# Optimization experiments

Measured on AMD Instinct MI355X. Metric: run time of the kernel, lower is better.

## Reference

```python
import jax, jax.numpy as jnp
import numpy as np

K_N = 20          # neighbors (init kwarg k_n)
EPS = 1e-5        # BN / InstanceNorm eps (torch default)


def _conv1x1(x, w, b):
    # x: [B,C,N,K], w: [O,C], b: [O]
    return jnp.einsum('bcnk,oc->bonk', x, w) + b[None, :, None, None]


def _bn(x, g, b):
    # training-mode BatchNorm2d: stats over (B,N,K)
    mean = x.mean(axis=(0, 2, 3), keepdims=True)
    var = x.var(axis=(0, 2, 3), keepdims=True)
    return (x - mean) * jax.lax.rsqrt(var + EPS) * g[None, :, None, None] + b[None, :, None, None]


def _inorm(x):
    # InstanceNorm2d (affine=False): stats over (N,K) per (b,c)
    mean = x.mean(axis=(2, 3), keepdims=True)
    var = x.var(axis=(2, 3), keepdims=True)
    return (x - mean) * jax.lax.rsqrt(var + EPS)


def _knn(x, k):
    # x: [B,C,N] -> idx [B,N,k] of nearest neighbors (excluding self)
    sq = jnp.sum(x * x, axis=1)                                   # [B,N]
    neg_d = 2.0 * jnp.einsum('bcn,bcm->bnm', x, x) - sq[:, :, None] - sq[:, None, :]
    _, idx = jax.lax.top_k(neg_d, k + 1)
    return idx[:, :, 1:]


def _res_block(x, w1, b1, g1, be1, w2, b2, g2, be2):
    # pre=False: residual branch is identity
    out = jax.nn.relu(_bn(_inorm(_conv1x1(x, w1, b1)), g1, be1))
    out = _bn(_inorm(_conv1x1(out, w2, b2)), g2, be2)
    return jax.nn.relu(out + x)


def _forward(data, conv0_w, conv0_b, bn0_g, bn0_b, lin_w, lin_b,
             res_w1, res_b1, res_g1, res_be1, res_w2, res_b2, res_g2, res_be2):
    B, C, N = data.shape
    # graph_feature: degree feature from normalized affinity matrix
    nrm = jnp.linalg.norm(data, axis=1, keepdims=True) + 1e-5
    o = data / nrm
    A = jnp.einsum('bcn,bcm->bnm', o, o)                          # [B,N,N]
    D = (jnp.sum(A, axis=1, keepdims=True) - 1.0) / N             # [B,1,N] (subtract eye diag)
    feat = jnp.concatenate([data, jax.nn.relu(jnp.tanh(D))], axis=1)  # [B,129,N]

    idx = _knn(feat, K_N)                                         # [B,N,k]
    xt = jnp.transpose(feat, (0, 2, 1))                           # [B,N,129]
    gathered = jax.vmap(lambda xb, ib: xb[ib])(xt, idx)           # [B,N,k,129]
    center = xt[:, :, None, :]
    edge = jnp.concatenate([jnp.broadcast_to(center, gathered.shape),
                            center - gathered], axis=3)           # [B,N,k,258]
    edge = jnp.transpose(edge, (0, 3, 1, 2))                      # [B,258,N,k]

    out = jax.nn.relu(_bn(_conv1x1(edge, conv0_w, conv0_b), bn0_g, bn0_b))
    out = jnp.max(out, axis=3, keepdims=True)                     # max_pool2d (1,k) -> [B,128,N,1]
    for i in range(4):
        out = _res_block(out, res_w1[i], res_b1[i], res_g1[i], res_be1[i],
                         res_w2[i], res_b2[i], res_g2[i], res_be2[i])
    logit = _conv1x1(out, lin_w, lin_b)                           # [B,1,N,1]
    return logit.reshape(logit.shape[0], -1)                      # [B,N]


def setup_inputs() -> dict:
    B, C, N = 8, 128, 2048
    key = jax.random.key(0)
    ks = jax.random.split(key, 10)
    s = 0.05
    return {
        'data': jax.random.normal(ks[0], (B, C, N), dtype=jnp.float32),
        'x': jax.random.normal(ks[1], (B, C, N), dtype=jnp.float32),  # unused by module
        'conv0_w': jax.random.normal(ks[2], (128, 258), dtype=jnp.float32) * s,
        'conv0_b': jnp.zeros((128,), dtype=jnp.float32),
        'bn0_g': jnp.ones((128,), dtype=jnp.float32),
        'bn0_b': jnp.zeros((128,), dtype=jnp.float32),
        'lin_w': jax.random.normal(ks[3], (1, 128), dtype=jnp.float32) * s,
        'lin_b': jnp.zeros((1,), dtype=jnp.float32),
        'res_w1': jax.random.normal(ks[4], (4, 128, 128), dtype=jnp.float32) * s,
        'res_b1': jnp.zeros((4, 128), dtype=jnp.float32),
        'res_g1': jnp.ones((4, 128), dtype=jnp.float32),
        'res_be1': jnp.zeros((4, 128), dtype=jnp.float32),
        'res_w2': jax.random.normal(ks[5], (4, 128, 128), dtype=jnp.float32) * s,
        'res_b2': jnp.zeros((4, 128), dtype=jnp.float32),
        'res_g2': jnp.ones((4, 128), dtype=jnp.float32),
        'res_be2': jnp.zeros((4, 128), dtype=jnp.float32),
    }


def reference(data, x, conv0_w, conv0_b, bn0_g, bn0_b, lin_w, lin_b,
              res_w1, res_b1, res_g1, res_be1, res_w2, res_b2, res_g2, res_be2):
    # x is accepted but unused, matching the torch module
    return _forward(data, conv0_w, conv0_b, bn0_g, bn0_b, lin_w, lin_b,
                    res_w1, res_b1, res_g1, res_be1, res_w2, res_b2, res_g2, res_be2)
```

## Files before the change

kernel.cpp:

```cpp
#include <hip/hip_runtime.h>
#include <math.h>
#include <float.h>

#define NB 8
#define NC 128
#define NN 2048
#define KNN 20
#define CF 129
#define CFP 144
#define EPSV 1e-5f

#define S_OFF      0
#define BN0S_OFF   1024
#define RESST_OFF  1280
#define NRM_OFF    17664
#define ZERO_CNT   34048
#define SQN_OFF    34048
#define WCAT_OFF   50432
#define FEAT_OFF   103936
#define PQ_OFF     2463232
#define X_OFF      6657536
#define SLOT_SZ    2097152
#define IDX_OFF    12948992
#define G_OFF      13276672
#define XB_OFF     46831104
#define WS_FLOATS  48928256
#define MMN_OFF    (X_OFF + SLOT_SZ)
#define MMX_OFF    (X_OFF + 2 * SLOT_SZ)

__launch_bounds__(256)
__global__ void k1a_sq(const float* __restrict__ data, float* __restrict__ ws) {
    int b = blockIdx.y;
    int n = blockIdx.x * 256 + threadIdx.x;
    int c0 = blockIdx.z * 32;
    const float* dp = data + (size_t)b * NC * NN + (size_t)c0 * NN + n;
    float acc = 0.f;
#pragma unroll
    for (int c = 0; c < 32; ++c) { float v = dp[(size_t)c * NN]; acc = fmaf(v, v, acc); }
    atomicAdd(&ws[NRM_OFF + b * NN + n], acc);
}

__launch_bounds__(256)
__global__ void k1s_colsum(const float* __restrict__ data, float* __restrict__ ws) {
    int b = blockIdx.y;
    int c0 = blockIdx.x * 16;
    int tid = threadIdx.x, w = tid >> 6, lane = tid & 63;
    __shared__ float Linv[NN];
    for (int r = tid; r < NN; r += 256)
        Linv[r] = 1.f / (sqrtf(ws[NRM_OFF + b * NN + r]) + 1e-5f);
    __syncthreads();
#pragma unroll
    for (int i = 0; i < 4; ++i) {
        int c = c0 + w * 4 + i;
        const float* dp = data + (size_t)b * NC * NN + (size_t)c * NN;
        float acc = 0.f;
        for (int n = lane; n < NN; n += 64) acc = fmaf(dp[n], Linv[n], acc);
        for (int off = 32; off; off >>= 1) acc += __shfl_down(acc, off);
        if (lane == 0) ws[S_OFF + b * NC + c] = acc;
    }
}

__launch_bounds__(256)
__global__ void k2_feat(const float* __restrict__ data, float* __restrict__ ws) {
    int b = blockIdx.y;
    int n0 = blockIdx.x * 64;
    int tid = threadIdx.x;
    __shared__ float Sb[NC];
    __shared__ __align__(16) float fT[64][CFP];
    __shared__ float redD[4][64], redQ[4][64];
    if (tid < NC) Sb[tid] = ws[S_OFF + b * NC + tid];
    __syncthreads();
    int nn = tid & 63, cg = tid >> 6;
    float dotp = 0.f, sq = 0.f;
    const float* dp = data + (size_t)b * NC * NN + n0 + nn;
    for (int c = cg; c < NC; c += 4) {
        float v = dp[(size_t)c * NN];
        fT[nn][c] = v;
        dotp += Sb[c] * v;
        sq += v * v;
    }
    redD[cg][nn] = dotp; redQ[cg][nn] = sq;
    __syncthreads();
    if (tid < 64) {
        float dt = redD[0][tid] + redD[1][tid] + redD[2][tid] + redD[3][tid];
        float sv = redQ[0][tid] + redQ[1][tid] + redQ[2][tid] + redQ[3][tid];
        float nrm = sqrtf(ws[NRM_OFF + b * NN + n0 + tid]) + 1e-5f;
        float D = (dt / nrm - 1.f) * (1.f / (float)NN);
        float f1 = tanhf(D); if (f1 < 0.f) f1 = 0.f;
        fT[tid][NC] = f1;
        for (int c = NC + 1; c < CFP; ++c) fT[tid][c] = 0.f;
        ws[SQN_OFF + b * NN + n0 + tid] = sv + f1 * f1;
    }
    __syncthreads();
    float* out = ws + FEAT_OFF + (size_t)(b * NN + n0) * CFP;
    for (int i = tid; i < 64 * CFP; i += 256) out[i] = ((float*)fT)[i];
}

__launch_bounds__(256)
__global__ void k4_wcat(const float* __restrict__ w, float* __restrict__ ws) {
    int i = blockIdx.x * 256 + threadIdx.x;
    int o = i / CFP, c = i % CFP;
    float v = 0.f;
    if (c < CF) {
        if (o < 128) v = w[o * 258 + c] + w[o * 258 + CF + c];
        else         v = w[(o - 128) * 258 + CF + c];
    }
    ws[WCAT_OFF + i] = v;
}

__launch_bounds__(256)
__global__ void k3_gram(float* __restrict__ ws) {
    __shared__ __align__(16) float As[8][128];
    __shared__ __align__(16) float Bs[8][128];
    int tid = threadIdx.x;
    int b = blockIdx.z;
    int m0 = blockIdx.x * 128, n0 = blockIdx.y * 128;
    const float* F = ws + FEAT_OFF + (size_t)b * NN * CFP;
    float acc[8][8];
#pragma unroll
    for (int i = 0; i < 8; ++i)
#pragma unroll
        for (int j = 0; j < 8; ++j) acc[i][j] = 0.f;
    int rr = tid >> 1, cq = tid & 1;
    int tx = tid & 15, ty = tid >> 4;
    for (int kc = 0; kc < CFP; kc += 8) {
        float4 av = *(const float4*)&F[(size_t)(n0 + rr) * CFP + kc + cq * 4];
        float4 bv = *(const float4*)&F[(size_t)(m0 + rr) * CFP + kc + cq * 4];
        __syncthreads();
        As[cq*4+0][rr] = av.x; As[cq*4+1][rr] = av.y; As[cq*4+2][rr] = av.z; As[cq*4+3][rr] = av.w;
        Bs[cq*4+0][rr] = bv.x; Bs[cq*4+1][rr] = bv.y; Bs[cq*4+2][rr] = bv.z; Bs[cq*4+3][rr] = bv.w;
        __syncthreads();
#pragma unroll
        for (int kk = 0; kk < 8; ++kk) {
            float a[8], bb[8];
            *(float4*)&a[0]  = *(const float4*)&As[kk][ty * 8];
            *(float4*)&a[4]  = *(const float4*)&As[kk][ty * 8 + 4];
            *(float4*)&bb[0] = *(const float4*)&Bs[kk][tx * 4];
            *(float4*)&bb[4] = *(const float4*)&Bs[kk][64 + tx * 4];
#pragma unroll
            for (int i = 0; i < 8; ++i)
#pragma unroll
                for (int j = 0; j < 8; ++j) acc[i][j] = fmaf(a[i], bb[j], acc[i][j]);
        }
    }
    float sqv[8];
#pragma unroll
    for (int j = 0; j < 4; ++j) {
        sqv[j]     = ws[SQN_OFF + b * NN + m0 + tx * 4 + j];
        sqv[4 + j] = ws[SQN_OFF + b * NN + m0 + 64 + tx * 4 + j];
    }
    float* G = ws + G_OFF + (size_t)b * NN * NN;
#pragma unroll
    for (int i = 0; i < 8; ++i) {
        int row = n0 + ty * 8 + i;
        float4 o1, o2;
        o1.x = 2.f*acc[i][0]-sqv[0]; o1.y = 2.f*acc[i][1]-sqv[1];
        o1.z = 2.f*acc[i][2]-sqv[2]; o1.w = 2.f*acc[i][3]-sqv[3];
        o2.x = 2.f*acc[i][4]-sqv[4]; o2.y = 2.f*acc[i][5]-sqv[5];
        o2.z = 2.f*acc[i][6]-sqv[6]; o2.w = 2.f*acc[i][7]-sqv[7];
        *(float4*)&G[(size_t)row * NN + m0 + tx * 4]      = o1;
        *(float4*)&G[(size_t)row * NN + m0 + 64 + tx * 4] = o2;
    }
}

__launch_bounds__(256)
__global__ void ksel(float* __restrict__ ws) {
    int wid = threadIdx.x >> 6, lane = threadIdx.x & 63;
    int r = blockIdx.x * 4 + wid;
    const float* row = ws + G_OFF + (size_t)r * NN;
    float v[32];
#pragma unroll
    for (int i = 0; i < 32; ++i) v[i] = row[lane + (i << 6)];
    float b1v = -FLT_MAX, b2v = -FLT_MAX;
    int b1i = 0, b2i = 0;
#pragma unroll
    for (int i = 0; i < 32; ++i) {
        float x = v[i];
        if (x > b1v)      { b2v = b1v; b2i = b1i; b1v = x; b1i = i; }
        else if (x > b2v) { b2v = x; b2i = i; }
    }
    unsigned int mask = 0u;
    bool has2 = true;
    int* out = (int*)(ws + IDX_OFF) + (size_t)r * KNN;
    for (int k = 0; k < 21; ++k) {
        float M = b1v;
#pragma unroll
        for (int off = 1; off < 64; off <<= 1) M = fmaxf(M, __shfl_xor(M, off));
        unsigned long long tied = __ballot(b1v == M);
        int mm;
        if (__popcll(tied) > 1) {
            int cand = (b1v == M) ? ((b1i << 6) | lane) : 0x7FFFFFFF;
#pragma unroll
            for (int off = 1; off < 64; off <<= 1) {
                int oc = __shfl_xor(cand, off);
                cand = oc < cand ? oc : cand;
            }
            mm = cand;
        } else {
            int l = __ffsll(tied) - 1;
            mm = (__shfl(b1i, l) << 6) | l;
        }
        if (k > 0 && lane == 0) out[k - 1] = mm;
        if (lane == (mm & 63)) {
            mask |= 1u << b1i;
            if (has2) { b1v = b2v; b1i = b2i; has2 = false; }
            else {
                b1v = -FLT_MAX; b2v = -FLT_MAX; b1i = 0; b2i = 0;
#pragma unroll
                for (int i = 0; i < 32; ++i) {
                    float x = (mask & (1u << i)) ? -FLT_MAX : v[i];
                    if (x > b1v)      { b2v = b1v; b2i = b1i; b1v = x; b1i = i; }
                    else if (x > b2v) { b2v = x; b2i = i; }
                }
                has2 = true;
            }
        }
    }
}

__launch_bounds__(256)
__global__ void k5_pq(float* __restrict__ ws) {
    __shared__ __align__(16) float As[16][64];
    __shared__ __align__(16) float Bs[16][64];
    int tid = threadIdx.x;
    int m0 = blockIdx.x * 64, o0 = blockIdx.y * 64;
    int rr = tid >> 2, cq = tid & 3;
    int tx = tid & 15, ty = tid >> 4;
    float acc[4][4];
#pragma unroll
    for (int i = 0; i < 4; ++i)
#pragma unroll
        for (int j = 0; j < 4; ++j) acc[i][j] = 0.f;
    const float* F  = ws + FEAT_OFF;
    const float* Wc = ws + WCAT_OFF;
    for (int kc = 0; kc < CFP; kc += 16) {
        float4 av = *(const float4*)&F [(size_t)(m0 + rr) * CFP + kc + cq * 4];
        float4 bv = *(const float4*)&Wc[(size_t)(o0 + rr) * CFP + kc + cq * 4];
        __syncthreads();
        As[cq*4+0][rr]=av.x; As[cq*4+1][rr]=av.y; As[cq*4+2][rr]=av.z; As[cq*4+3][rr]=av.w;
        Bs[cq*4+0][rr]=bv.x; Bs[cq*4+1][rr]=bv.y; Bs[cq*4+2][rr]=bv.z; Bs[cq*4+3][rr]=bv.w;
        __syncthreads();
#pragma unroll
        for (int kk = 0; kk < 16; ++kk) {
            float a[4], bb[4];
            *(float4*)&a[0]  = *(const float4*)&As[kk][ty * 4];
            *(float4*)&bb[0] = *(const float4*)&Bs[kk][tx * 4];
#pragma unroll
            for (int i = 0; i < 4; ++i)
#pragma unroll
                for (int j = 0; j < 4; ++j) acc[i][j] = fmaf(a[i], bb[j], acc[i][j]);
        }
    }
#pragma unroll
    for (int i = 0; i < 4; ++i) {
        float4 o;
        o.x = acc[i][0]; o.y = acc[i][1]; o.z = acc[i][2]; o.w = acc[i][3];
        *(float4*)&ws[PQ_OFF + (size_t)(m0 + ty * 4 + i) * 256 + o0 + tx * 4] = o;
    }
}

__launch_bounds__(256)
__global__ void k6_bn0stats(float* __restrict__ ws) {
    int tid = threadIdx.x;
    int o = tid & 127, h = tid >> 7;
    int m0 = blockIdx.x * 16;
    const float* PQ = ws + PQ_OFF;
    const int* idx = (const int*)(ws + IDX_OFF);
    float* MMn = ws + MMN_OFF;
    float* MMx = ws + MMX_OFF;
    __shared__ float red[2][128];
    float s = 0.f, q = 0.f;
    for (int p = h; p < 16; p += 2) {
        int m = m0 + p;
        int bb = m >> 11;
        float pv = PQ[(size_t)m * 256 + o];
        const int* ip = idx + (size_t)m * KNN;
        float mn = FLT_MAX, mx = -FLT_MAX;
        for (int k = 0; k < KNN; ++k) {
            int j = ip[k];
            float val = pv - PQ[(size_t)(bb * NN + j) * 256 + 128 + o];
            s += val; q += val * val;
            mn = fminf(mn, val); mx = fmaxf(mx, val);
        }
        MMn[(size_t)m * NC + o] = mn;
        MMx[(size_t)m * NC + o] = mx;
    }
    red[h][o] = s; __syncthreads();
    if (tid < 128) atomicAdd(&ws[BN0S_OFF + tid], red[0][tid] + red[1][tid]);
    __syncthreads();
    red[h][o] = q; __syncthreads();
    if (tid < 128) atomicAdd(&ws[BN0S_OFF + 128 + tid], red[0][tid] + red[1][tid]);
}

__launch_bounds__(256)
__global__ void k8_apply(float* __restrict__ ws, const float* __restrict__ g,
                         const float* __restrict__ be) {
    int e = blockIdx.x * 256 + threadIdx.x;
    int fi = e * 4;
    int o = fi & 127;
    const float cnt = 1.f / (float)(NB * NN * KNN);
    float4 sum4 = *(const float4*)&ws[BN0S_OFF + o];
    float4 ssq4 = *(const float4*)&ws[BN0S_OFF + 128 + o];
    float4 g4   = *(const float4*)&g[o];
    float4 be4  = *(const float4*)&be[o];
    float4 mn = *(const float4*)&ws[MMN_OFF + fi];
    float4 mx = *(const float4*)&ws[MMX_OFF + fi];
    float4 r;
#define BN0_DO(comp) { \
    float m_ = sum4.comp * cnt; \
    float v_ = ssq4.comp * cnt - m_ * m_; if (v_ < 0.f) v_ = 0.f; \
    float sc_ = g4.comp * rsqrtf(v_ + EPSV); \
    float sh_ = be4.comp - m_ * sc_; \
    r.comp = fmaxf(fmaf(sc_ > 0.f ? mx.comp : mn.comp, sc_, sh_), 0.f); }
    BN0_DO(x) BN0_DO(y) BN0_DO(z) BN0_DO(w)
#undef BN0_DO
    *(float4*)&ws[X_OFF + fi] = r;
}

__launch_bounds__(256)
__global__ void k9f_conv(const float* __restrict__ x, const float* __restrict__ w,
                         float* __restrict__ y, float* __restrict__ stats,
                         const float* __restrict__ statsIn,
                         const float* __restrict__ g, const float* __restrict__ be,
                         const float* __restrict__ xin, float* __restrict__ xw) {
    __shared__ __align__(16) float As[16][64];
    __shared__ __align__(16) float Bs[16][64];
    __shared__ float red[16][64];
    __shared__ float vvv[8][128];
    __shared__ float scs[128], shs[128];
    int tid = threadIdx.x;
    int m0 = blockIdx.x * 64, o0 = blockIdx.y * 64;
    int bA = m0 >> 11;
    if (statsIn) {
        for (int e = tid; e < 1024; e += 256) {
            float sum = statsIn[e], ssq = statsIn[1024 + e];
            float m_ = sum * (1.f / (float)NN);
            float v_ = ssq * (1.f / (float)NN) - m_ * m_; if (v_ < 0.f) v_ = 0.f;
            vvv[e >> 7][e & 127] = v_ / (v_ + EPSV);
        }
        __syncthreads();
        if (tid < 128) {
            float a = 0.f;
#pragma unroll
            for (int b2 = 0; b2 < NB; ++b2) a += vvv[b2][tid];
            float rsbn = rsqrtf(a * (1.f / (float)NB) + EPSV);
            float sum = statsIn[bA * 128 + tid], ssq = statsIn[1024 + bA * 128 + tid];
            float m_ = sum * (1.f / (float)NN);
            float v_ = ssq * (1.f / (float)NN) - m_ * m_; if (v_ < 0.f) v_ = 0.f;
            float sc_ = rsqrtf(v_ + EPSV) * rsbn * g[tid];
            scs[tid] = sc_;
            shs[tid] = be[tid] - m_ * sc_;
        }
        __syncthreads();
    }
    int rr = tid >> 2, cq = tid & 3;
    int tx = tid & 15, ty = tid >> 4;
    float acc[4][4];
#pragma unroll
    for (int i = 0; i < 4; ++i)
#pragma unroll
        for (int j = 0; j < 4; ++j) acc[i][j] = 0.f;
    for (int kc = 0; kc < NC; kc += 16) {
        float4 av = *(const float4*)&x[(size_t)(m0 + rr) * NC + kc + cq * 4];
        if (statsIn) {
            int c = kc + cq * 4;
            av.x = fmaf(av.x, scs[c],     shs[c]);
            av.y = fmaf(av.y, scs[c + 1], shs[c + 1]);
            av.z = fmaf(av.z, scs[c + 2], shs[c + 2]);
            av.w = fmaf(av.w, scs[c + 3], shs[c + 3]);
            if (xin) {
                float4 xv = *(const float4*)&xin[(size_t)(m0 + rr) * NC + kc + cq * 4];
                av.x += xv.x; av.y += xv.y; av.z += xv.z; av.w += xv.w;
            }
            av.x = fmaxf(av.x, 0.f); av.y = fmaxf(av.y, 0.f);
            av.z = fmaxf(av.z, 0.f); av.w = fmaxf(av.w, 0.f);
            if (xw && blockIdx.y == 0)
                *(float4*)&xw[(size_t)(m0 + rr) * NC + kc + cq * 4] = av;
        }
        float4 bv = *(const float4*)&w[(size_t)(o0 + rr) * NC + kc + cq * 4];
        __syncthreads();
        As[cq*4+0][rr]=av.x; As[cq*4+1][rr]=av.y; As[cq*4+2][rr]=av.z; As[cq*4+3][rr]=av.w;
        Bs[cq*4+0][rr]=bv.x; Bs[cq*4+1][rr]=bv.y; Bs[cq*4+2][rr]=bv.z; Bs[cq*4+3][rr]=bv.w;
        __syncthreads();
#pragma unroll
        for (int kk = 0; kk < 16; ++kk) {
            float a[4], bb[4];
            *(float4*)&a[0]  = *(const float4*)&As[kk][ty * 4];
            *(float4*)&bb[0] = *(const float4*)&Bs[kk][tx * 4];
#pragma unroll
            for (int i = 0; i < 4; ++i)
#pragma unroll
                for (int j = 0; j < 4; ++j) acc[i][j] = fmaf(a[i], bb[j], acc[i][j]);
        }
    }
#pragma unroll
    for (int i = 0; i < 4; ++i) {
        float4 o;
        o.x = acc[i][0]; o.y = acc[i][1]; o.z = acc[i][2]; o.w = acc[i][3];
        *(float4*)&y[(size_t)(m0 + ty * 4 + i) * NC + o0 + tx * 4] = o;
    }
    float s[4], q[4];
#pragma unroll
    for (int j = 0; j < 4; ++j) {
        s[j] = acc[0][j] + acc[1][j] + acc[2][j] + acc[3][j];
        q[j] = acc[0][j]*acc[0][j] + acc[1][j]*acc[1][j] + acc[2][j]*acc[2][j] + acc[3][j]*acc[3][j];
    }
    *(float4*)&red[ty][tx * 4] = make_float4(s[0], s[1], s[2], s[3]);
    __syncthreads();
    if (tid < 64) {
        float t = 0.f;
#pragma unroll
        for (int g2 = 0; g2 < 16; ++g2) t += red[g2][tid];
        atomicAdd(&stats[bA * NC + o0 + tid], t);
    }
    __syncthreads();
    *(float4*)&red[ty][tx * 4] = make_float4(q[0], q[1], q[2], q[3]);
    __syncthreads();
    if (tid < 64) {
        float t = 0.f;
#pragma unroll
        for (int g2 = 0; g2 < 16; ++g2) t += red[g2][tid];
        atomicAdd(&stats[1024 + bA * NC + o0 + tid], t);
    }
}

__launch_bounds__(256)
__global__ void k12_logit(const float* __restrict__ y2, const float* __restrict__ xin,
                          const float* __restrict__ statsIn,
                          const float* __restrict__ g, const float* __restrict__ be,
                          const float* __restrict__ lw, const float* __restrict__ lb,
                          float* __restrict__ out) {
    __shared__ float wsh[128];
    __shared__ float vvv[8][128];
    __shared__ float scs[128], shs[128];
    int tid = threadIdx.x;
    int b = (blockIdx.x * 256) >> 11;
    if (tid < 128) wsh[tid] = lw[tid];
    for (int e = tid; e < 1024; e += 256) {
        float sum = statsIn[e], ssq = statsIn[1024 + e];
        float m_ = sum * (1.f / (float)NN);
        float v_ = ssq * (1.f / (float)NN) - m_ * m_; if (v_ < 0.f) v_ = 0.f;
        vvv[e >> 7][e & 127] = v_ / (v_ + EPSV);
    }
    __syncthreads();
    if (tid < 128) {
        float a = 0.f;
#pragma unroll
        for (int b2 = 0; b2 < NB; ++b2) a += vvv[b2][tid];
        float rsbn = rsqrtf(a * (1.f / (float)NB) + EPSV);
        float sum = statsIn[b * 128 + tid], ssq = statsIn[1024 + b * 128 + tid];
        float m_ = sum * (1.f / (float)NN);
        float v_ = ssq * (1.f / (float)NN) - m_ * m_; if (v_ < 0.f) v_ = 0.f;
        float sc_ = rsqrtf(v_ + EPSV) * rsbn * g[tid];
        scs[tid] = sc_;
        shs[tid] = be[tid] - m_ * sc_;
    }
    __syncthreads();
    int m = blockIdx.x * 256 + tid;
    const float* yp = y2 + (size_t)m * NC;
    const float* xp = xin + (size_t)m * NC;
    float acc = lb[0];
    for (int c = 0; c < NC; c += 4) {
        float4 yv = *(const float4*)&yp[c];
        float4 xv = *(const float4*)&xp[c];
        float v0 = fmaxf(fmaf(yv.x, scs[c],     shs[c])     + xv.x, 0.f);
        float v1 = fmaxf(fmaf(yv.y, scs[c + 1], shs[c + 1]) + xv.y, 0.f);
        float v2 = fmaxf(fmaf(yv.z, scs[c + 2], shs[c + 2]) + xv.z, 0.f);
        float v3 = fmaxf(fmaf(yv.w, scs[c + 3], shs[c + 3]) + xv.w, 0.f);
        acc += v0 * wsh[c] + v1 * wsh[c + 1] + v2 * wsh[c + 2] + v3 * wsh[c + 3];
    }
    out[m] = acc;
}

extern "C" void kernel_launch(void* const* d_in, const int* in_sizes, int n_in,
                              void* d_out, int out_size, void* d_ws, size_t ws_size,
                              hipStream_t stream) {
    if (ws_size < (size_t)WS_FLOATS * 4) return;
    const float* data    = (const float*)d_in[0];
    const float* conv0_w = (const float*)d_in[2];
    const float* bn0_g   = (const float*)d_in[4];
    const float* bn0_b   = (const float*)d_in[5];
    const float* lin_w   = (const float*)d_in[6];
    const float* lin_b   = (const float*)d_in[7];
    const float* res_w1  = (const float*)d_in[8];
    const float* res_g1  = (const float*)d_in[10];
    const float* res_be1 = (const float*)d_in[11];
    const float* res_w2  = (const float*)d_in[12];
    const float* res_g2  = (const float*)d_in[14];
    const float* res_be2 = (const float*)d_in[15];
    float* ws  = (float*)d_ws;
    float* out = (float*)d_out;

    hipMemsetAsync(d_ws, 0, ZERO_CNT * sizeof(float), stream);
    k1a_sq<<<dim3(8, 8, 4), 256, 0, stream>>>(data, ws);
    k1s_colsum<<<dim3(8, 8), 256, 0, stream>>>(data, ws);
    k2_feat<<<dim3(32, 8), 256, 0, stream>>>(data, ws);
    k4_wcat<<<144, 256, 0, stream>>>(conv0_w, ws);
    k3_gram<<<dim3(16, 16, 8), 256, 0, stream>>>(ws);
    ksel<<<4096, 256, 0, stream>>>(ws);
    k5_pq<<<dim3(256, 4), 256, 0, stream>>>(ws);
    k6_bn0stats<<<1024, 256, 0, stream>>>(ws);
    k8_apply<<<2048, 256, 0, stream>>>(ws, bn0_g, bn0_b);

    float* XA = ws + X_OFF;
    float* Y1 = ws + X_OFF + SLOT_SZ;
    float* Y2 = ws + X_OFF + 2 * SLOT_SZ;
    float* XB = ws + XB_OFF;
    float* ST = ws + RESST_OFF;

    k9f_conv<<<dim3(256, 2), 256, 0, stream>>>(XA, res_w1, Y1, ST,
                                               nullptr, nullptr, nullptr, nullptr, nullptr);
    k9f_conv<<<dim3(256, 2), 256, 0, stream>>>(Y1, res_w2, Y2, ST + 2048,
                                               ST, res_g1, res_be1, nullptr, nullptr);
    float* xcur = XA; float* xnext = XB;
    for (int i = 1; i < 4; ++i) {
        int L = 2 * i, L2 = 2 * i + 1;
        k9f_conv<<<dim3(256, 2), 256, 0, stream>>>(Y2, res_w1 + i * 16384, Y1, ST + L * 2048,
                                                   ST + (L - 1) * 2048,
                                                   res_g2 + (i - 1) * 128, res_be2 + (i - 1) * 128,
                                                   xcur, xnext);
        k9f_conv<<<dim3(256, 2), 256, 0, stream>>>(Y1, res_w2 + i * 16384, Y2, ST + L2 * 2048,
                                                   ST + L * 2048,
                                                   res_g1 + i * 128, res_be1 + i * 128,
                                                   nullptr, nullptr);
        float* t = xcur; xcur = xnext; xnext = t;
    }
    k12_logit<<<64, 256, 0, stream>>>(Y2, xcur, ST + 7 * 2048, res_g2 + 3 * 128, res_be2 + 3 * 128,
                                      lin_w, lin_b, out);
}
```

Before: 441.0 us.

## Split 129th feature channel out as rank-1 term and fuse norm/colsum kernels

The padded 144-wide feature matrix is replaced by a 128-wide one, with the extra tanh degree channel stored separately and added as a rank-1 correction in the gram and PQ GEMM epilogues. This cuts the GEMM reduction depth and the feature memory traffic. The squared-norm and column-sum kernels are merged into one tiled kernel, and the top-k selection now loads rows with contiguous float4 accesses under a changed index encoding. The main risks are the extra epilogue loads and the correctness of the new index mapping.

```diff
diff --git a/kernel.cpp b/kernel.cpp
--- a/kernel.cpp
+++ b/kernel.cpp
@@ -6,18 +6,18 @@
 #define NC 128
 #define NN 2048
 #define KNN 20
-#define CF 129
-#define CFP 144
 #define EPSV 1e-5f
 
 #define S_OFF      0
 #define BN0S_OFF   1024
 #define RESST_OFF  1280
+#define ZERO_CNT   17664
 #define NRM_OFF    17664
-#define ZERO_CNT   34048
 #define SQN_OFF    34048
-#define WCAT_OFF   50432
-#define FEAT_OFF   103936
+#define F1_OFF     50432
+#define WCAT_OFF   66816
+#define WCOL_OFF   99584
+#define F128_OFF   99840
 #define PQ_OFF     2463232
 #define X_OFF      6657536
 #define SLOT_SZ    2097152
@@ -29,34 +29,34 @@
 #define MMX_OFF    (X_OFF + 2 * SLOT_SZ)
 
 __launch_bounds__(256)
-__global__ void k1a_sq(const float* __restrict__ data, float* __restrict__ ws) {
+__global__ void k1_fused(const float* __restrict__ data, float* __restrict__ ws) {
     int b = blockIdx.y;
-    int n = blockIdx.x * 256 + threadIdx.x;
-    int c0 = blockIdx.z * 32;
-    const float* dp = data + (size_t)b * NC * NN + (size_t)c0 * NN + n;
-    float acc = 0.f;
-#pragma unroll
-    for (int c = 0; c < 32; ++c) { float v = dp[(size_t)c * NN]; acc = fmaf(v, v, acc); }
-    atomicAdd(&ws[NRM_OFF + b * NN + n], acc);
-}
-
-__launch_bounds__(256)
-__global__ void k1s_colsum(const float* __restrict__ data, float* __restrict__ ws) {
-    int b = blockIdx.y;
-    int c0 = blockIdx.x * 16;
-    int tid = threadIdx.x, w = tid >> 6, lane = tid & 63;
-    __shared__ float Linv[NN];
-    for (int r = tid; r < NN; r += 256)
-        Linv[r] = 1.f / (sqrtf(ws[NRM_OFF + b * NN + r]) + 1e-5f);
-    __syncthreads();
-#pragma unroll
-    for (int i = 0; i < 4; ++i) {
-        int c = c0 + w * 4 + i;
-        const float* dp = data + (size_t)b * NC * NN + (size_t)c * NN;
-        float acc = 0.f;
-        for (int n = lane; n < NN; n += 64) acc = fmaf(dp[n], Linv[n], acc);
-        for (int off = 32; off; off >>= 1) acc += __shfl_down(acc, off);
-        if (lane == 0) ws[S_OFF + b * NC + c] = acc;
+    int n0 = blockIdx.x * 64;
+    int tid = threadIdx.x;
+    __shared__ float tile[128][65];
+    __shared__ float red[4][64];
+    __shared__ float Linv[64];
+    int g = tid >> 6, nn = tid & 63;
+    const float* dp = data + (size_t)b * NC * NN + n0 + nn;
+    float sq = 0.f;
+    for (int c = g; c < 128; c += 4) {
+        float v = dp[(size_t)c * NN];
+        tile[c][nn] = v;
+        sq = fmaf(v, v, sq);
+    }
+    red[g][nn] = sq;
+    __syncthreads();
+    if (tid < 64) {
+        float s = red[0][tid] + red[1][tid] + red[2][tid] + red[3][tid];
+        ws[NRM_OFF + b * NN + n0 + tid] = s;
+        Linv[tid] = 1.f / (sqrtf(s) + 1e-5f);
+    }
+    __syncthreads();
+    if (tid < 128) {
+        float s = 0.f;
+#pragma unroll 8
+        for (int j = 0; j < 64; ++j) s = fmaf(tile[tid][j], Linv[j], s);
+        atomicAdd(&ws[S_OFF + b * NC + tid], s);
     }
 }
 
@@ -66,46 +66,48 @@
     int n0 = blockIdx.x * 64;
     int tid = threadIdx.x;
     __shared__ float Sb[NC];
-    __shared__ __align__(16) float fT[64][CFP];
-    __shared__ float redD[4][64], redQ[4][64];
+    __shared__ float fT[64][129];
+    __shared__ float redD[4][64];
     if (tid < NC) Sb[tid] = ws[S_OFF + b * NC + tid];
     __syncthreads();
     int nn = tid & 63, cg = tid >> 6;
-    float dotp = 0.f, sq = 0.f;
+    float dotp = 0.f;
     const float* dp = data + (size_t)b * NC * NN + n0 + nn;
     for (int c = cg; c < NC; c += 4) {
         float v = dp[(size_t)c * NN];
         fT[nn][c] = v;
-        dotp += Sb[c] * v;
-        sq += v * v;
-    }
-    redD[cg][nn] = dotp; redQ[cg][nn] = sq;
+        dotp = fmaf(Sb[c], v, dotp);
+    }
+    redD[cg][nn] = dotp;
     __syncthreads();
     if (tid < 64) {
         float dt = redD[0][tid] + redD[1][tid] + redD[2][tid] + redD[3][tid];
-        float sv = redQ[0][tid] + redQ[1][tid] + redQ[2][tid] + redQ[3][tid];
-        float nrm = sqrtf(ws[NRM_OFF + b * NN + n0 + tid]) + 1e-5f;
+        float nrmsq = ws[NRM_OFF + b * NN + n0 + tid];
+        float nrm = sqrtf(nrmsq) + 1e-5f;
         float D = (dt / nrm - 1.f) * (1.f / (float)NN);
         float f1 = tanhf(D); if (f1 < 0.f) f1 = 0.f;
-        fT[tid][NC] = f1;
-        for (int c = NC + 1; c < CFP; ++c) fT[tid][c] = 0.f;
-        ws[SQN_OFF + b * NN + n0 + tid] = sv + f1 * f1;
-    }
-    __syncthreads();
-    float* out = ws + FEAT_OFF + (size_t)(b * NN + n0) * CFP;
-    for (int i = tid; i < 64 * CFP; i += 256) out[i] = ((float*)fT)[i];
+        ws[F1_OFF + b * NN + n0 + tid] = f1;
+        ws[SQN_OFF + b * NN + n0 + tid] = nrmsq + f1 * f1;
+    }
+    __syncthreads();
+    float* out = ws + F128_OFF + (size_t)(b * NN + n0) * 128;
+    for (int i = tid; i < 64 * 128; i += 256) out[i] = fT[i >> 7][i & 127];
 }
 
 __launch_bounds__(256)
 __global__ void k4_wcat(const float* __restrict__ w, float* __restrict__ ws) {
     int i = blockIdx.x * 256 + threadIdx.x;
-    int o = i / CFP, c = i % CFP;
-    float v = 0.f;
-    if (c < CF) {
-        if (o < 128) v = w[o * 258 + c] + w[o * 258 + CF + c];
-        else         v = w[(o - 128) * 258 + CF + c];
-    }
-    ws[WCAT_OFF + i] = v;
+    if (i < 32768) {
+        int o = i >> 7, c = i & 127;
+        float v = (o < 128) ? w[o * 258 + c] + w[o * 258 + 129 + c]
+                            : w[(o - 128) * 258 + 129 + c];
+        ws[WCAT_OFF + i] = v;
+    } else if (i < 33024) {
+        int o = i - 32768;
+        float v = (o < 128) ? w[o * 258 + 128] + w[o * 258 + 257]
+                            : w[(o - 128) * 258 + 257];
+        ws[WCOL_OFF + o] = v;
+    }
 }
 
 __launch_bounds__(256)
@@ -115,7 +117,7 @@
     int tid = threadIdx.x;
     int b = blockIdx.z;
     int m0 = blockIdx.x * 128, n0 = blockIdx.y * 128;
-    const float* F = ws + FEAT_OFF + (size_t)b * NN * CFP;
+    const float* F = ws + F128_OFF + (size_t)b * NN * 128;
     float acc[8][8];
 #pragma unroll
     for (int i = 0; i < 8; ++i)
@@ -123,9 +125,9 @@
         for (int j = 0; j < 8; ++j) acc[i][j] = 0.f;
     int rr = tid >> 1, cq = tid & 1;
     int tx = tid & 15, ty = tid >> 4;
-    for (int kc = 0; kc < CFP; kc += 8) {
-        float4 av = *(const float4*)&F[(size_t)(n0 + rr) * CFP + kc + cq * 4];
-        float4 bv = *(const float4*)&F[(size_t)(m0 + rr) * CFP + kc + cq * 4];
+    for (int kc = 0; kc < 128; kc += 8) {
+        float4 av = *(const float4*)&F[(size_t)(n0 + rr) * 128 + kc + cq * 4];
+        float4 bv = *(const float4*)&F[(size_t)(m0 + rr) * 128 + kc + cq * 4];
         __syncthreads();
         As[cq*4+0][rr] = av.x; As[cq*4+1][rr] = av.y; As[cq*4+2][rr] = av.z; As[cq*4+3][rr] = av.w;
         Bs[cq*4+0][rr] = bv.x; Bs[cq*4+1][rr] = bv.y; Bs[cq*4+2][rr] = bv.z; Bs[cq*4+3][rr] = bv.w;
@@ -143,21 +145,29 @@
                 for (int j = 0; j < 8; ++j) acc[i][j] = fmaf(a[i], bb[j], acc[i][j]);
         }
     }
-    float sqv[8];
+    float sqv[8], f1m[8];
+    const float* F1 = ws + F1_OFF + b * NN;
 #pragma unroll
     for (int j = 0; j < 4; ++j) {
         sqv[j]     = ws[SQN_OFF + b * NN + m0 + tx * 4 + j];
         sqv[4 + j] = ws[SQN_OFF + b * NN + m0 + 64 + tx * 4 + j];
+        f1m[j]     = F1[m0 + tx * 4 + j];
+        f1m[4 + j] = F1[m0 + 64 + tx * 4 + j];
     }
     float* G = ws + G_OFF + (size_t)b * NN * NN;
 #pragma unroll
     for (int i = 0; i < 8; ++i) {
         int row = n0 + ty * 8 + i;
+        float f1n = F1[row];
         float4 o1, o2;
-        o1.x = 2.f*acc[i][0]-sqv[0]; o1.y = 2.f*acc[i][1]-sqv[1];
-        o1.z = 2.f*acc[i][2]-sqv[2]; o1.w = 2.f*acc[i][3]-sqv[3];
-        o2.x = 2.f*acc[i][4]-sqv[4]; o2.y = 2.f*acc[i][5]-sqv[5];
-        o2.z = 2.f*acc[i][6]-sqv[6]; o2.w = 2.f*acc[i][7]-sqv[7];
+        o1.x = 2.f*fmaf(f1n, f1m[0], acc[i][0]) - sqv[0];
+        o1.y = 2.f*fmaf(f1n, f1m[1], acc[i][1]) - sqv[1];
+        o1.z = 2.f*fmaf(f1n, f1m[2], acc[i][2]) - sqv[2];
+        o1.w = 2.f*fmaf(f1n, f1m[3], acc[i][3]) - sqv[3];
+        o2.x = 2.f*fmaf(f1n, f1m[4], acc[i][4]) - sqv[4];
+        o2.y = 2.f*fmaf(f1n, f1m[5], acc[i][5]) - sqv[5];
+        o2.z = 2.f*fmaf(f1n, f1m[6], acc[i][6]) - sqv[6];
+        o2.w = 2.f*fmaf(f1n, f1m[7], acc[i][7]) - sqv[7];
         *(float4*)&G[(size_t)row * NN + m0 + tx * 4]      = o1;
         *(float4*)&G[(size_t)row * NN + m0 + 64 + tx * 4] = o2;
     }
@@ -170,7 +180,8 @@
     const float* row = ws + G_OFF + (size_t)r * NN;
     float v[32];
 #pragma unroll
-    for (int i = 0; i < 32; ++i) v[i] = row[lane + (i << 6)];
+    for (int i = 0; i < 8; ++i)
+        *(float4*)&v[i * 4] = *(const float4*)&row[lane * 32 + i * 4];
     float b1v = -FLT_MAX, b2v = -FLT_MAX;
     int b1i = 0, b2i = 0;
 #pragma unroll
@@ -189,7 +200,7 @@
         unsigned long long tied = __ballot(b1v == M);
         int mm;
         if (__popcll(tied) > 1) {
-            int cand = (b1v == M) ? ((b1i << 6) | lane) : 0x7FFFFFFF;
+            int cand = (b1v == M) ? ((lane << 5) | b1i) : 0x7FFFFFFF;
 #pragma unroll
             for (int off = 1; off < 64; off <<= 1) {
                 int oc = __shfl_xor(cand, off);
@@ -198,10 +209,10 @@
             mm = cand;
         } else {
             int l = __ffsll(tied) - 1;
-            mm = (__shfl(b1i, l) << 6) | l;
+            mm = (l << 5) | __shfl(b1i, l);
         }
         if (k > 0 && lane == 0) out[k - 1] = mm;
-        if (lane == (mm & 63)) {
+        if (lane == (mm >> 5)) {
             mask |= 1u << b1i;
             if (has2) { b1v = b2v; b1i = b2i; has2 = false; }
             else {
@@ -231,11 +242,11 @@
     for (int i = 0; i < 4; ++i)
 #pragma unroll
         for (int j = 0; j < 4; ++j) acc[i][j] = 0.f;
-    const float* F  = ws + FEAT_OFF;
+    const float* F  = ws + F128_OFF;
     const float* Wc = ws + WCAT_OFF;
-    for (int kc = 0; kc < CFP; kc += 16) {
-        float4 av = *(const float4*)&F [(size_t)(m0 + rr) * CFP + kc + cq * 4];
-        float4 bv = *(const float4*)&Wc[(size_t)(o0 + rr) * CFP + kc + cq * 4];
+    for (int kc = 0; kc < 128; kc += 16) {
+        float4 av = *(const float4*)&F [(size_t)(m0 + rr) * 128 + kc + cq * 4];
+        float4 bv = *(const float4*)&Wc[(size_t)(o0 + rr) * 128 + kc + cq * 4];
         __syncthreads();
         As[cq*4+0][rr]=av.x; As[cq*4+1][rr]=av.y; As[cq*4+2][rr]=av.z; As[cq*4+3][rr]=av.w;
         Bs[cq*4+0][rr]=bv.x; Bs[cq*4+1][rr]=bv.y; Bs[cq*4+2][rr]=bv.z; Bs[cq*4+3][rr]=bv.w;
@@ -251,10 +262,19 @@
                 for (int j = 0; j < 4; ++j) acc[i][j] = fmaf(a[i], bb[j], acc[i][j]);
         }
     }
+    float wc[4], f1v[4];
+#pragma unroll
+    for (int j = 0; j < 4; ++j) {
+        wc[j]  = ws[WCOL_OFF + o0 + tx * 4 + j];
+        f1v[j] = ws[F1_OFF + m0 + ty * 4 + j];
+    }
 #pragma unroll
     for (int i = 0; i < 4; ++i) {
         float4 o;
-        o.x = acc[i][0]; o.y = acc[i][1]; o.z = acc[i][2]; o.w = acc[i][3];
+        o.x = fmaf(f1v[i], wc[0], acc[i][0]);
+        o.y = fmaf(f1v[i], wc[1], acc[i][1]);
+        o.z = fmaf(f1v[i], wc[2], acc[i][2]);
+        o.w = fmaf(f1v[i], wc[3], acc[i][3]);
         *(float4*)&ws[PQ_OFF + (size_t)(m0 + ty * 4 + i) * 256 + o0 + tx * 4] = o;
     }
 }
@@ -492,10 +512,9 @@
     float* out = (float*)d_out;
 
     hipMemsetAsync(d_ws, 0, ZERO_CNT * sizeof(float), stream);
-    k1a_sq<<<dim3(8, 8, 4), 256, 0, stream>>>(data, ws);
-    k1s_colsum<<<dim3(8, 8), 256, 0, stream>>>(data, ws);
+    k1_fused<<<dim3(32, 8), 256, 0, stream>>>(data, ws);
     k2_feat<<<dim3(32, 8), 256, 0, stream>>>(data, ws);
-    k4_wcat<<<144, 256, 0, stream>>>(conv0_w, ws);
+    k4_wcat<<<130, 256, 0, stream>>>(conv0_w, ws);
     k3_gram<<<dim3(16, 16, 8), 256, 0, stream>>>(ws);
     ksel<<<4096, 256, 0, stream>>>(ws);
     k5_pq<<<dim3(256, 4), 256, 0, stream>>>(ws);
```

Measured after the change: 407.5 us. 1.08x faster.
